# Kernel tuning notes

Measured on AMD Instinct MI355X. Metric: run time of the kernel, lower is better.

## Reference

```python
import jax, jax.numpy as jnp
import numpy as np
from jax import lax

B = 512          # scoring batch size
NC = 10          # n_classes
N_LAB = 256      # int(B * plb), plb = 0.5 (labeled indices are the first N_LAB)
TOL = 1e-3       # gtg_t
MAX_ITER = 30    # gtg_i
INTERM = 128
CH = [64, 128, 256, 512]
SZ = [32, 16, 8, 4]
EMB = 512


def setup_inputs() -> dict:
    key = jax.random.key(0)
    ks = jax.random.split(key, 16)
    inp = {}
    for i, (c, s) in enumerate(zip(CH, SZ)):
        inp["feat%d" % i] = jax.random.normal(ks[i], (B, c, s, s), jnp.float32)
        inp["conv_w%d" % i] = jax.random.normal(ks[4 + i], (c, c, 3, 3), jnp.float32) * 0.05
        inp["conv_b%d" % i] = jnp.zeros((c,), jnp.float32)
        inp["bn_g%d" % i] = jnp.ones((c,), jnp.float32)
        inp["bn_b%d" % i] = jnp.zeros((c,), jnp.float32)
        inp["lin_w%d" % i] = jax.random.normal(ks[8 + i], (INTERM, c), jnp.float32) * 0.05
        inp["lin_b%d" % i] = jnp.zeros((INTERM,), jnp.float32)
    inp["fin_w"] = jax.random.normal(ks[12], (1, 4 * INTERM), jnp.float32) * 0.05
    inp["fin_b"] = jnp.zeros((1,), jnp.float32)
    inp["embedds"] = jax.random.normal(ks[13], (B, EMB), jnp.float32)
    inp["labels"] = jax.random.randint(ks[14], (B,), 0, NC)
    return inp


def _branch(x, cw, cb, g, b, lw, lb):
    # Conv3x3(same) -> BatchNorm (train mode, batch stats, eps=1e-5) -> ReLU -> GAP -> Linear -> ReLU
    y = lax.conv_general_dilated(x, cw, (1, 1), 'SAME',
                                 dimension_numbers=('NCHW', 'OIHW', 'NCHW')) + cb[None, :, None, None]
    m = y.mean(axis=(0, 2, 3), keepdims=True)
    v = ((y - m) ** 2).mean(axis=(0, 2, 3), keepdims=True)  # biased variance (train-mode BN)
    y = jax.nn.relu(g[None, :, None, None] * (y - m) * lax.rsqrt(v + 1e-5) + b[None, :, None, None])
    y = y.mean(axis=(2, 3))  # AvgPool2d(feature_size) == global average pool -> [B, C]
    return jax.nn.relu(y @ lw.T + lb)


def _gtg(E, labels):
    # get_A_e_d: pairwise euclidean distances clamped to [0.1, 1.0]
    sq = jnp.sum(E * E, axis=1)
    d2 = jnp.maximum(sq[:, None] + sq[None, :] - 2.0 * (E @ E.T), 0.0)
    A0 = jnp.clip(jnp.sqrt(d2), 0.1, 1.0)
    # rbf kernel: 7th nearest neighbor (ascending for 'e_d') gives per-sample sigma
    seventh = E[jnp.argsort(A0, axis=1)[:, 6]]
    sig = jnp.clip(jnp.sqrt(jnp.sum((E - seventh) ** 2, axis=1)), 0.1, 1.0)
    A = jnp.clip(jnp.exp(-(A0 ** 2) / (sig[:, None] * sig[None, :])), 0.0, 1.0)
    # threshold strategy 'mean' with AM_function == 'e_d': A = where(A > mean(A), 1, A)
    A = jnp.where(A > A.mean(), 1.0, A)
    # AM_strategy 'mixed' with 'e_d': flip only the labeled x labeled block
    A = A.at[:N_LAB, :N_LAB].set(1.0 - A[:N_LAB, :N_LAB])
    # get_X: one-hot for labeled (first N_LAB), uniform 1/NC for unlabeled
    X0 = jnp.concatenate([jax.nn.one_hot(labels[:N_LAB], NC, dtype=jnp.float32),
                          jnp.full((B - N_LAB, NC), 1.0 / NC, jnp.float32)], axis=0)
    hist0 = jnp.zeros((B, MAX_ITER), jnp.float32)

    def cond(c):
        return (c[3] > TOL) & (c[2] < MAX_ITER)

    def body(c):
        X, h, i, _ = c
        Xn = X * (A @ X)
        Xn = Xn / jnp.sum(Xn, axis=1, keepdims=True)
        ent = -jnp.sum(jnp.where(Xn > 0, Xn * jnp.log(Xn), 0.0), axis=1)
        h = lax.dynamic_update_slice(h, ent[:, None], (0, i))
        return (Xn, h, i + 1, jnp.linalg.norm(Xn - X))

    X, h, _, _ = lax.while_loop(cond, body, (X0, hist0, jnp.int32(0), jnp.float32(jnp.inf)))
    return h.mean(axis=1), X  # ent_strategy == 'mean'


def reference(feat0, feat1, feat2, feat3,
              conv_w0, conv_b0, bn_g0, bn_b0, lin_w0, lin_b0,
              conv_w1, conv_b1, bn_g1, bn_b1, lin_w1, lin_b1,
              conv_w2, conv_b2, bn_g2, bn_b2, lin_w2, lin_b2,
              conv_w3, conv_b3, bn_g3, bn_b3, lin_w3, lin_b3,
              fin_w, fin_b, embedds, labels):
    o0 = _branch(feat0, conv_w0, conv_b0, bn_g0, bn_b0, lin_w0, lin_b0)
    o1 = _branch(feat1, conv_w1, conv_b1, bn_g1, bn_b1, lin_w1, lin_b1)
    o2 = _branch(feat2, conv_w2, conv_b2, bn_g2, bn_b2, lin_w2, lin_b2)
    o3 = _branch(feat3, conv_w3, conv_b3, bn_g3, bn_b3, lin_w3, lin_b3)
    y_pred = (jnp.concatenate([o0, o1, o2, o3], axis=1) @ fin_w.T + fin_b)[:, 0]
    y_true, X = _gtg(embedds, labels)
    labeled_mask = jnp.arange(B) < N_LAB
    return (y_pred, y_true, X, labeled_mask)
```

## Files before the change

kernel.cpp:

```cpp
#include <hip/hip_runtime.h>
#include <hip/hip_bf16.h>
#include <math.h>

static constexpr int kNC = 10;
static constexpr int kNLab = 256;
static constexpr int kMaxIter = 30;

using short8 = __attribute__((ext_vector_type(8))) short;
using f32x4  = __attribute__((ext_vector_type(4))) float;

__device__ __forceinline__ unsigned short f2bf(float f) {
  unsigned int u = __float_as_uint(f);
  u += 0x7FFFu + ((u >> 16) & 1u);
  return (unsigned short)(u >> 16);
}
__device__ __forceinline__ float bf2f(unsigned short u) {
  return __uint_as_float(((unsigned int)u) << 16);
}

template <int C, int S>
__global__ __launch_bounds__(256) void xpack_kernel(const float* __restrict__ x,
                                                    unsigned short* __restrict__ xp) {
  __shared__ float t[C][S + 1];
  const int n = blockIdx.x / S, h = blockIdx.x % S;
  const float* src = x + (size_t)n * C * S * S;
  for (int e = threadIdx.x; e < C * S; e += 256) {
    int c = e / S, w = e % S;
    t[c][w] = src[((size_t)c * S + h) * S + w];
  }
  __syncthreads();
  unsigned short* dst = xp + ((size_t)(n * S + h) * S) * C;
  for (int e = threadIdx.x; e < C * S; e += 256) {
    int w = e / C, c = e % C;
    dst[(size_t)w * C + c] = f2bf(t[c][w]);
  }
}

__global__ void wpack_all(const float* __restrict__ w0, const float* __restrict__ w1,
                          const float* __restrict__ w2, const float* __restrict__ w3,
                          unsigned short* __restrict__ wpk) {
  int idx = blockIdx.x * 256 + threadIdx.x;
  if (idx >= 3133440) return;
  const float* w; int C, off;
  if (idx < 36864)        { w = w0; C = 64;  off = 0; }
  else if (idx < 184320)  { w = w1; C = 128; off = 36864; }
  else if (idx < 774144)  { w = w2; C = 256; off = 184320; }
  else                    { w = w3; C = 512; off = 774144; }
  int e = idx - off;
  int CO16T = C / 16, CIK = C / 32;
  int e8 = e & 7, l = (e >> 3) & 63;
  int rest = e >> 9;
  int co16 = rest % CO16T;
  int rest2 = rest / CO16T;
  int cik = rest2 % CIK, tap = rest2 / CIK;
  int co = co16 * 16 + (l & 15);
  int ci = cik * 32 + (l >> 4) * 8 + e8;
  wpk[idx] = f2bf(w[((size_t)co * C + ci) * 9 + tap]);
}

template <int C, int S, int NI, int NR, int WV, int BF, int MODE>
__global__ __launch_bounds__(WV * 64)
void conv_mfma(const unsigned short* __restrict__ xp, const unsigned short* __restrict__ wpk,
               const float* __restrict__ bias, unsigned short* __restrict__ y,
               float* __restrict__ psum, float* __restrict__ psq, int npart, int partBase,
               const float* __restrict__ scale, const float* __restrict__ shift,
               float* __restrict__ pp, int pxGlobalBase) {
  constexpr int SS = S * S;
  constexpr int PXB = NI * NR * S;
  constexpr int TPB = WV * 64;
  constexpr int HR = NR + 2, HC = S + 2;
  constexpr int CIK = C / 32, CO16T = C / 16;
  constexpr int UNITS = NI * HR * HC * 4;
  constexpr int NU = (UNITS + TPB - 1) / TPB;
  static_assert(WV * BF * 16 == PXB, "wave px mismatch");
  static_assert(MODE != 2 || BF == 4, "MODE2 assumes 64px/wave");
  __shared__ __align__(16) char xs[NI * HR * HC * 80];

  const int tid = threadIdx.x;
  const int wv = tid >> 6, l = tid & 63, l15 = l & 15, l4 = l >> 4;
  const int coblk = blockIdx.y;
  const int co_base = coblk * 64;
  const int pxb = blockIdx.x * PXB;
  const int n_t = pxb / SS;
  const int r0 = (pxb % SS) / S;

  int pxoff[BF];
#pragma unroll
  for (int bf = 0; bf < BF; ++bf) {
    int pxloc = wv * (BF * 16) + bf * 16 + l15;
    int ii = pxloc / (NR * S);
    int rr = (pxloc % (NR * S)) / S;
    int cc = pxloc % S;
    pxoff[bf] = ((ii * HR + rr) * HC + cc) * 80 + l4 * 16;
  }

  f32x4 acc[4][BF];
#pragma unroll
  for (int a = 0; a < 4; ++a)
#pragma unroll
    for (int b = 0; b < BF; ++b) acc[a][b] = (f32x4){0.f, 0.f, 0.f, 0.f};

  uint4 vreg[NU];
  auto loadU = [&](int cik) {
#pragma unroll
    for (int k = 0; k < NU; ++k) {
      int u = tid + k * TPB;
      uint4 v = {0u, 0u, 0u, 0u};
      if (u < UNITS) {
        int k16 = u & 3;
        int t = u >> 2;
        int hc = t % HC;
        int t2 = t / HC;
        int hr = t2 % HR;
        int ii = t2 / HR;
        int row = r0 + hr - 1, col = hc - 1;
        if (row >= 0 && row < S && col >= 0 && col < S)
          v = *(const uint4*)(xp + ((size_t)((n_t + ii) * S + row) * S + col) * C + cik * 32 + k16 * 8);
      }
      vreg[k] = v;
    }
  };

  loadU(0);
  for (int cik = 0; cik < CIK; ++cik) {
    __syncthreads();
#pragma unroll
    for (int k = 0; k < NU; ++k) {
      int u = tid + k * TPB;
      if (u < UNITS) *(uint4*)(xs + (u >> 2) * 80 + (u & 3) * 16) = vreg[k];
    }
    __syncthreads();
    if (cik + 1 < CIK) loadU(cik + 1);
#pragma unroll
    for (int tap = 0; tap < 9; ++tap) {
      const int tapoff = ((tap / 3) * HC + (tap % 3)) * 80;
      short8 wf[4], xf[BF];
#pragma unroll
      for (int af = 0; af < 4; ++af)
        wf[af] = *(const short8*)(wpk + ((size_t)((tap * CIK + cik) * CO16T + coblk * 4 + af) * 64 + l) * 8);
#pragma unroll
      for (int bf = 0; bf < BF; ++bf)
        xf[bf] = *(const short8*)(xs + pxoff[bf] + tapoff);
#pragma unroll
      for (int af = 0; af < 4; ++af)
#pragma unroll
        for (int bf = 0; bf < BF; ++bf)
          acc[af][bf] = __builtin_amdgcn_mfma_f32_16x16x32_bf16(wf[af], xf[bf], acc[af][bf], 0, 0, 0);
    }
  }

#pragma unroll
  for (int af = 0; af < 4; ++af) {
    const int co0 = co_base + af * 16 + l4 * 4;
    float4 bv = *(const float4*)(bias + co0);
    float s[4] = {0.f, 0.f, 0.f, 0.f}, q[4] = {0.f, 0.f, 0.f, 0.f};
    float4 sc4, sh4;
    if (MODE == 2) {
      sc4 = *(const float4*)(scale + co0);
      sh4 = *(const float4*)(shift + co0);
    }
#pragma unroll
    for (int bf = 0; bf < BF; ++bf) {
      float o[4];
#pragma unroll
      for (int r = 0; r < 4; ++r) o[r] = acc[af][bf][r] + ((const float*)&bv)[r];
      if (MODE == 0) {
        ushort4 pk;
        pk.x = f2bf(o[0]); pk.y = f2bf(o[1]); pk.z = f2bf(o[2]); pk.w = f2bf(o[3]);
        size_t px = (size_t)(pxb + wv * (BF * 16) + bf * 16 + l15);
        *(ushort4*)(y + px * C + co0) = pk;
      }
      if (MODE == 2) {
#pragma unroll
        for (int r = 0; r < 4; ++r)
          s[r] += fmaxf(fmaf(((const float*)&sc4)[r], o[r], ((const float*)&sh4)[r]), 0.f);
      } else {
#pragma unroll
        for (int r = 0; r < 4; ++r) { s[r] += o[r]; q[r] += o[r] * o[r]; }
      }
    }
#pragma unroll
    for (int m = 1; m < 16; m <<= 1) {
#pragma unroll
      for (int r = 0; r < 4; ++r) {
        s[r] += __shfl_xor(s[r], m);
        if (MODE != 2) q[r] += __shfl_xor(q[r], m);
      }
    }
    if (l15 == 0) {
      if (MODE == 2) {
        int n = (pxGlobalBase + pxb) / SS;
        int qw = ((pxGlobalBase + pxb) % SS) / 64 + wv;
#pragma unroll
        for (int r = 0; r < 4; ++r)
          pp[((size_t)(n * C + co0 + r)) * 16 + qw] = s[r];
      } else {
        int part = partBase + blockIdx.x * WV + wv;
#pragma unroll
        for (int r = 0; r < 4; ++r) {
          psum[(size_t)(co0 + r) * npart + part] = s[r];
          psq[(size_t)(co0 + r) * npart + part] = q[r];
        }
      }
    }
  }
}

__global__ __launch_bounds__(256)
void stats2_kernel(const float* __restrict__ psum, const float* __restrict__ psq,
                   const float* __restrict__ g, const float* __restrict__ bb,
                   float* __restrict__ scale, float* __restrict__ shift,
                   int npart, float invN) {
  int c = blockIdx.x;
  __shared__ float rs[256], rq[256];
  float s = 0.f, q = 0.f;
  for (int p = threadIdx.x; p < npart; p += 256) {
    s += psum[(size_t)c * npart + p];
    q += psq[(size_t)c * npart + p];
  }
  rs[threadIdx.x] = s; rq[threadIdx.x] = q;
  __syncthreads();
  for (int st = 128; st; st >>= 1) {
    if (threadIdx.x < st) { rs[threadIdx.x] += rs[threadIdx.x + st]; rq[threadIdx.x] += rq[threadIdx.x + st]; }
    __syncthreads();
  }
  if (threadIdx.x == 0) {
    float m = rs[0] * invN;
    float v = rq[0] * invN - m * m;
    float sc = g[c] / sqrtf(v + 1e-5f);
    scale[c] = sc;
    shift[c] = bb[c] - m * sc;
  }
}

template <int C, int S>
__global__ __launch_bounds__(256)
void pool_nhwc(const unsigned short* __restrict__ y, const float* __restrict__ scale,
               const float* __restrict__ shift, float* __restrict__ pooled) {
  constexpr int SS = S * S;
  int n = blockIdx.x;
  const unsigned short* yr = y + (size_t)n * SS * C;
  if (C >= 256) {
    for (int co = threadIdx.x; co < C; co += 256) {
      float sc = scale[co], sh = shift[co], s = 0.f;
      for (int p = 0; p < SS; ++p) s += fmaxf(fmaf(sc, bf2f(yr[(size_t)p * C + co]), sh), 0.f);
      pooled[(size_t)n * C + co] = s * (1.f / SS);
    }
  } else {
    constexpr int G = 256 / C;
    int co = threadIdx.x % C;
    int sl = threadIdx.x / C;
    float sc = scale[co], sh = shift[co], s = 0.f;
    for (int p = sl; p < SS; p += G) s += fmaxf(fmaf(sc, bf2f(yr[(size_t)p * C + co]), sh), 0.f);
    __shared__ float red[256];
    red[threadIdx.x] = s;
    __syncthreads();
    if (threadIdx.x < C) {
      float t = 0.f;
      for (int gg = 0; gg < G; ++gg) t += red[gg * C + co];
      pooled[(size_t)n * C + co] = t * (1.f / SS);
    }
  }
}

__global__ void poolfin_kernel(const float* __restrict__ pp, float* __restrict__ pooled) {
  int i = blockIdx.x * 256 + threadIdx.x;
  if (i >= 512 * 64) return;
  float s = 0.f;
  for (int qn = 0; qn < 16; ++qn) s += pp[(size_t)i * 16 + qn];
  pooled[i] = s * (1.f / 1024.f);
}

__global__ void lin_kernel(const float* __restrict__ pooled, const float* __restrict__ lw,
                           const float* __restrict__ lb, float* __restrict__ oc,
                           int C, int brOff) {
  int idx = blockIdx.x * 256 + threadIdx.x;
  if (idx >= 512 * 128) return;
  int j = idx & 127, n = idx >> 7;
  const float4* pr = (const float4*)(pooled + (size_t)n * C);
  const float4* wr = (const float4*)(lw + (size_t)j * C);
  float s = 0.f;
  for (int t = 0; t < C / 4; ++t) {
    float4 a = pr[t], b = wr[t];
    s += a.x * b.x + a.y * b.y + a.z * b.z + a.w * b.w;
  }
  s += lb[j];
  oc[n * 512 + brOff + j] = fmaxf(s, 0.f);
}

__global__ void ypred_kernel(const float* __restrict__ oc, const float* __restrict__ fw,
                             const float* __restrict__ fb, float* __restrict__ out) {
  int wv = threadIdx.x >> 6, l = threadIdx.x & 63;
  int n = blockIdx.x * 4 + wv;
  float s = 0.f;
  for (int k = l; k < 512; k += 64) s += oc[n * 512 + k] * fw[k];
#pragma unroll
  for (int m = 32; m; m >>= 1) s += __shfl_down(s, m);
  if (l == 0) out[n] = s + fb[0];
}

__global__ void sqnorm_kernel(const float* __restrict__ E, float* __restrict__ sq) {
  int wv = threadIdx.x >> 6, l = threadIdx.x & 63;
  int n = blockIdx.x * 4 + wv;
  const float* row = E + (size_t)n * 512;
  float s = 0.f;
  for (int k = l; k < 512; k += 64) { float v = row[k]; s += v * v; }
#pragma unroll
  for (int m = 32; m; m >>= 1) s += __shfl_down(s, m);
  if (l == 0) sq[n] = s;
}

__global__ __launch_bounds__(256) void a0_kernel(const float* __restrict__ E,
                                                 const float* __restrict__ sq,
                                                 float* __restrict__ A0) {
  int bi = blockIdx.x / 32, bj = blockIdx.x % 32;
  int ti = threadIdx.x % 16, tj = threadIdx.x / 16;
  __shared__ float Ei[16][68], Ej[16][68];
  float acc = 0.f;
  for (int k0 = 0; k0 < 512; k0 += 64) {
    for (int e = threadIdx.x; e < 1024; e += 256) {
      int rr = e >> 6, cc = e & 63;
      Ei[rr][cc] = E[(size_t)(bi * 16 + rr) * 512 + k0 + cc];
      Ej[rr][cc] = E[(size_t)(bj * 16 + rr) * 512 + k0 + cc];
    }
    __syncthreads();
#pragma unroll 16
    for (int kk = 0; kk < 64; ++kk) acc = fmaf(Ei[tj][kk], Ej[ti][kk], acc);
    __syncthreads();
  }
  int i = bi * 16 + tj, j = bj * 16 + ti;
  float d2 = fmaxf(sq[i] + sq[j] - 2.f * acc, 0.f);
  A0[(size_t)i * 512 + j] = fminf(fmaxf(sqrtf(d2), 0.1f), 1.0f);
}

__global__ void seventh_kernel(const float* __restrict__ A0, int* __restrict__ idx7) {
  int i = blockIdx.x * 256 + threadIdx.x;
  if (i >= 512) return;
  float v[7]; int ix[7];
#pragma unroll
  for (int t = 0; t < 7; ++t) { v[t] = 3.4e38f; ix[t] = 0; }
  const float* row = A0 + (size_t)i * 512;
  for (int j = 0; j < 512; ++j) {
    float a = row[j];
    if (a < v[6]) {
      int pos = 6;
      while (pos > 0 && a < v[pos - 1]) { v[pos] = v[pos - 1]; ix[pos] = ix[pos - 1]; --pos; }
      v[pos] = a; ix[pos] = j;
    }
  }
  idx7[i] = ix[6];
}

__global__ void sig_kernel(const float* __restrict__ E, const int* __restrict__ idx7,
                           float* __restrict__ sig) {
  int wv = threadIdx.x >> 6, l = threadIdx.x & 63;
  int n = blockIdx.x * 4 + wv;
  const float* r1 = E + (size_t)n * 512;
  const float* r2 = E + (size_t)idx7[n] * 512;
  float s = 0.f;
  for (int k = l; k < 512; k += 64) { float d = r1[k] - r2[k]; s += d * d; }
#pragma unroll
  for (int m = 32; m; m >>= 1) s += __shfl_down(s, m);
  if (l == 0) sig[n] = fminf(fmaxf(sqrtf(s), 0.1f), 1.0f);
}

__global__ void aexp_kernel(const float* __restrict__ A0, const float* __restrict__ sig,
                            float* __restrict__ A, float* __restrict__ part) {
  int t = blockIdx.x * 256 + threadIdx.x;
  int base = t * 4;
  int i = base >> 9, j0 = base & 511;
  float si = sig[i];
  float4 a = *(const float4*)(A0 + base);
  float4 o;
  o.x = fminf(fmaxf(expf(-a.x * a.x / (si * sig[j0 + 0])), 0.f), 1.f);
  o.y = fminf(fmaxf(expf(-a.y * a.y / (si * sig[j0 + 1])), 0.f), 1.f);
  o.z = fminf(fmaxf(expf(-a.z * a.z / (si * sig[j0 + 2])), 0.f), 1.f);
  o.w = fminf(fmaxf(expf(-a.w * a.w / (si * sig[j0 + 3])), 0.f), 1.f);
  *(float4*)(A + base) = o;
  float lsum = o.x + o.y + o.z + o.w;
#pragma unroll
  for (int m = 32; m; m >>= 1) lsum += __shfl_down(lsum, m);
  __shared__ float sred[4];
  if ((threadIdx.x & 63) == 0) sred[threadIdx.x >> 6] = lsum;
  __syncthreads();
  if (threadIdx.x == 0) part[blockIdx.x] = sred[0] + sred[1] + sred[2] + sred[3];
}

__global__ void meanred_kernel(const float* __restrict__ part, float* __restrict__ meanA) {
  if (threadIdx.x == 0 && blockIdx.x == 0) {
    float s = 0.f;
    for (int p = 0; p < 256; ++p) s += part[p];
    meanA[0] = s * (1.0f / 262144.0f);
  }
}

__global__ void thresh_kernel(float* __restrict__ A, const float* __restrict__ meanA) {
  int t = blockIdx.x * 256 + threadIdx.x;
  int base = t * 4;
  int i = base >> 9, j0 = base & 511;
  float m = meanA[0];
  float4 v = *(const float4*)(A + base);
  v.x = v.x > m ? 1.f : v.x;
  v.y = v.y > m ? 1.f : v.y;
  v.z = v.z > m ? 1.f : v.z;
  v.w = v.w > m ? 1.f : v.w;
  if (i < kNLab && j0 < kNLab) {
    v.x = 1.f - v.x; v.y = 1.f - v.y; v.z = 1.f - v.z; v.w = 1.f - v.w;
  }
  *(float4*)(A + base) = v;
}

__device__ __forceinline__ void gridbar(int* cnt, int* sense, int ph) {
  __syncthreads();
  if (threadIdx.x == 0) {
    __threadfence();
    if (__hip_atomic_fetch_add(cnt, 1, __ATOMIC_ACQ_REL, __HIP_MEMORY_SCOPE_AGENT) == 63) {
      __hip_atomic_store(cnt, 0, __ATOMIC_RELAXED, __HIP_MEMORY_SCOPE_AGENT);
      __hip_atomic_store(sense, ph, __ATOMIC_RELEASE, __HIP_MEMORY_SCOPE_AGENT);
    } else {
      while (__hip_atomic_load(sense, __ATOMIC_ACQUIRE, __HIP_MEMORY_SCOPE_AGENT) < ph)
        __builtin_amdgcn_s_sleep(2);
    }
  }
  __syncthreads();
}

__global__ __launch_bounds__(256)
void gtg_iters(const float* __restrict__ A, const int* __restrict__ labels,
               float* __restrict__ Xa, float* __restrict__ Xb,
               float* __restrict__ hist, float* __restrict__ diffPart,
               float* __restrict__ out, int* __restrict__ bar) {
  constexpr int NB = 64;
  const int b = blockIdx.x, tid = threadIdx.x;
  const int wv = tid >> 6, l = tid & 63;
  __shared__ float Xs[512 * kNC];
  __shared__ float red[4];
  int* cnt = bar; int* sense = bar + 1;
  int ph = 0;

  for (int e = tid; e < 8 * kNC; e += 256) {
    int r = b * 8 + e / kNC, c = e % kNC;
    Xa[r * kNC + c] = (r < kNLab) ? ((labels[r] == c) ? 1.f : 0.f) : 0.1f;
  }
  for (int e = tid; e < 8 * kMaxIter; e += 256)
    hist[(size_t)(b * 8 + e / kMaxIter) * kMaxIter + e % kMaxIter] = 0.f;
  gridbar(cnt, sense, ++ph);

  float* Xin = Xa;
  float* Xout = Xb;
  int it = 0;
  for (; it < kMaxIter; ++it) {
    if (it > 0) {
      float s = 0.f;
      for (int p = 0; p < NB; ++p) s += diffPart[(it - 1) * NB + p];
      if (sqrtf(s) <= 0.001f) break;
    }
    for (int e = tid; e < 512 * kNC; e += 256) Xs[e] = Xin[e];
    __syncthreads();
    float dpw = 0.f;
    for (int rr = 0; rr < 2; ++rr) {
      int i = b * 8 + wv * 2 + rr;
      const float* Ar = A + (size_t)i * 512;
      float ax[kNC];
#pragma unroll
      for (int c = 0; c < kNC; ++c) ax[c] = 0.f;
      for (int j = l; j < 512; j += 64) {
        float a = Ar[j];
        const float* xr = Xs + j * kNC;
#pragma unroll
        for (int c = 0; c < kNC; ++c) ax[c] = fmaf(a, xr[c], ax[c]);
      }
#pragma unroll
      for (int c = 0; c < kNC; ++c)
#pragma unroll
        for (int m = 32; m; m >>= 1) ax[c] += __shfl_xor(ax[c], m);
      if (l == 0) {
        float xn[kNC], ssum = 0.f;
#pragma unroll
        for (int c = 0; c < kNC; ++c) { xn[c] = Xs[i * kNC + c] * ax[c]; ssum += xn[c]; }
        float ent = 0.f, dp = 0.f;
#pragma unroll
        for (int c = 0; c < kNC; ++c) {
          float xv = xn[c] / ssum;
          if (xv > 0.f) ent -= xv * logf(xv);
          float d = xv - Xs[i * kNC + c];
          dp += d * d;
          Xout[i * kNC + c] = xv;
        }
        hist[(size_t)i * kMaxIter + it] = ent;
        dpw += dp;
      }
    }
    if (l == 0) red[wv] = dpw;
    __syncthreads();
    if (tid == 0) diffPart[it * NB + b] = red[0] + red[1] + red[2] + red[3];
    gridbar(cnt, sense, ++ph);
    float* tmp = Xin; Xin = Xout; Xout = tmp;
  }

  if (tid < 8) {
    int i = b * 8 + tid;
    float s = 0.f;
    for (int t = 0; t < kMaxIter; ++t) s += hist[(size_t)i * kMaxIter + t];
    out[512 + i] = s * (1.0f / 30.0f);
    out[6144 + i] = (i < kNLab) ? 1.0f : 0.0f;
  }
  for (int e = tid; e < 80; e += 256) out[1024 + b * 80 + e] = Xin[b * 80 + e];
}

extern "C" void kernel_launch(void* const* d_in, const int* in_sizes, int n_in,
                              void* d_out, int out_size, void* d_ws, size_t ws_size,
                              hipStream_t stream) {
  (void)in_sizes; (void)n_in; (void)out_size;

  const float* feat[4]; const float* cw[4]; const float* cbp[4];
  const float* bg[4]; const float* bbp[4]; const float* lw[4]; const float* lbp[4];
  for (int b = 0; b < 4; ++b) {
    int base = b * 7;
    feat[b] = (const float*)d_in[base + 0];
    cw[b]  = (const float*)d_in[base + 1];
    cbp[b] = (const float*)d_in[base + 2];
    bg[b]  = (const float*)d_in[base + 3];
    bbp[b] = (const float*)d_in[base + 4];
    lw[b]  = (const float*)d_in[base + 5];
    lbp[b] = (const float*)d_in[base + 6];
  }
  const float* finw = (const float*)d_in[28];
  const float* finb = (const float*)d_in[29];
  const float* emb  = (const float*)d_in[30];
  const int* labels = (const int*)d_in[31];
  float* out = (float*)d_out;

  float* wsf = (float*)d_ws;
  unsigned short* xpad = (unsigned short*)wsf;
  unsigned short* yP   = (unsigned short*)(wsf + 4194304);
  unsigned short* wpk  = (unsigned short*)(wsf + 12582912);
  size_t off = 14149632;
  float* psum = wsf + off; off += 524288;
  float* psq  = wsf + off; off += 524288;
  float* pp   = wsf + off; off += 524288;
  float* scale = wsf + off; off += 512;
  float* shift = wsf + off; off += 512;
  float* pooled = wsf + off; off += 491520;
  float* oc = wsf + off; off += 262144;
  float* sq = wsf + off; off += 512;
  float* A0 = wsf + off; off += 262144;
  float* Am = wsf + off; off += 262144;
  float* sig = wsf + off; off += 512;
  int* idx7 = (int*)(wsf + off); off += 512;
  float* meanPart = wsf + off; off += 256;
  float* meanA = wsf + off; off += 4;
  float* X0 = wsf + off; off += 5120;
  float* X1 = wsf + off; off += 5120;
  float* hist = wsf + off; off += 15360;
  float* diffPart = wsf + off; off += 1920;
  int* bar = (int*)(wsf + off); off += 4;
  size_t yb0_off = off;
  unsigned short* yB0 = (unsigned short*)(wsf + yb0_off);
  const bool bigB0 = ws_size >= (yb0_off + 16777216) * sizeof(float);

  unsigned short* wpkB[4] = {wpk, wpk + 36864, wpk + 184320, wpk + 774144};

  wpack_all<<<(3133440 + 255) / 256, 256, 0, stream>>>(cw[0], cw[1], cw[2], cw[3], wpk);

  for (int c = 0; c < 2; ++c) {
    xpack_kernel<128, 16><<<256 * 16, 256, 0, stream>>>(feat[1] + (size_t)c * 8388608, xpad);
    conv_mfma<128, 16, 1, 8, 4, 2, 0><<<dim3(512, 2), 256, 0, stream>>>(
        xpad, wpkB[1], cbp[1], yP + (size_t)c * 8388608, psum, psq, 4096, c * 2048,
        nullptr, nullptr, nullptr, 0);
  }
  stats2_kernel<<<128, 256, 0, stream>>>(psum, psq, bg[1], bbp[1], scale, shift, 4096, 1.f / 131072.f);
  pool_nhwc<128, 16><<<512, 256, 0, stream>>>(yP, scale, shift, pooled + 32768);
  lin_kernel<<<256, 256, 0, stream>>>(pooled + 32768, lw[1], lbp[1], oc, 128, 128);

  xpack_kernel<256, 8><<<512 * 8, 256, 0, stream>>>(feat[2], xpad);
  conv_mfma<256, 8, 2, 8, 4, 2, 0><<<dim3(256, 4), 256, 0, stream>>>(
      xpad, wpkB[2], cbp[2], yP, psum, psq, 1024, 0, nullptr, nullptr, nullptr, 0);
  stats2_kernel<<<256, 256, 0, stream>>>(psum, psq, bg[2], bbp[2], scale, shift, 1024, 1.f / 32768.f);
  pool_nhwc<256, 8><<<512, 256, 0, stream>>>(yP, scale, shift, pooled + 98304);
  lin_kernel<<<256, 256, 0, stream>>>(pooled + 98304, lw[2], lbp[2], oc, 256, 256);

  xpack_kernel<512, 4><<<512 * 4, 256, 0, stream>>>(feat[3], xpad);
  conv_mfma<512, 4, 8, 4, 4, 2, 0><<<dim3(64, 8), 256, 0, stream>>>(
      xpad, wpkB[3], cbp[3], yP, psum, psq, 256, 0, nullptr, nullptr, nullptr, 0);
  stats2_kernel<<<512, 256, 0, stream>>>(psum, psq, bg[3], bbp[3], scale, shift, 256, 1.f / 8192.f);
  pool_nhwc<512, 4><<<512, 256, 0, stream>>>(yP, scale, shift, pooled + 229376);
  lin_kernel<<<256, 256, 0, stream>>>(pooled + 229376, lw[3], lbp[3], oc, 512, 384);

  if (bigB0) {
    for (int c = 0; c < 4; ++c) {
      xpack_kernel<64, 32><<<128 * 32, 256, 0, stream>>>(feat[0] + (size_t)c * 8388608, xpad);
      conv_mfma<64, 32, 1, 8, 4, 4, 0><<<dim3(512, 1), 256, 0, stream>>>(
          xpad, wpkB[0], cbp[0], yB0 + (size_t)c * 8388608, psum, psq, 8192, c * 2048,
          nullptr, nullptr, nullptr, 0);
    }
    stats2_kernel<<<64, 256, 0, stream>>>(psum, psq, bg[0], bbp[0], scale, shift, 8192, 1.f / 524288.f);
    pool_nhwc<64, 32><<<512, 256, 0, stream>>>(yB0, scale, shift, pooled);
  } else {
    for (int c = 0; c < 4; ++c) {
      xpack_kernel<64, 32><<<128 * 32, 256, 0, stream>>>(feat[0] + (size_t)c * 8388608, xpad);
      conv_mfma<64, 32, 1, 8, 4, 4, 1><<<dim3(512, 1), 256, 0, stream>>>(
          xpad, wpkB[0], cbp[0], nullptr, psum, psq, 8192, c * 2048, nullptr, nullptr, nullptr, 0);
    }
    stats2_kernel<<<64, 256, 0, stream>>>(psum, psq, bg[0], bbp[0], scale, shift, 8192, 1.f / 524288.f);
    for (int c = 0; c < 4; ++c) {
      xpack_kernel<64, 32><<<128 * 32, 256, 0, stream>>>(feat[0] + (size_t)c * 8388608, xpad);
      conv_mfma<64, 32, 1, 8, 4, 4, 2><<<dim3(512, 1), 256, 0, stream>>>(
          xpad, wpkB[0], cbp[0], nullptr, nullptr, nullptr, 0, 0, scale, shift, pp, c * 131072);
    }
    poolfin_kernel<<<128, 256, 0, stream>>>(pp, pooled);
  }
  lin_kernel<<<256, 256, 0, stream>>>(pooled, lw[0], lbp[0], oc, 64, 0);

  ypred_kernel<<<128, 256, 0, stream>>>(oc, finw, finb, out);
  sqnorm_kernel<<<128, 256, 0, stream>>>(emb, sq);
  a0_kernel<<<1024, 256, 0, stream>>>(emb, sq, A0);
  seventh_kernel<<<2, 256, 0, stream>>>(A0, idx7);
  sig_kernel<<<128, 256, 0, stream>>>(emb, idx7, sig);
  aexp_kernel<<<256, 256, 0, stream>>>(A0, sig, Am, meanPart);
  meanred_kernel<<<1, 64, 0, stream>>>(meanPart, meanA);
  thresh_kernel<<<256, 256, 0, stream>>>(Am, meanA);

  hipMemsetAsync(bar, 0, 8, stream);
  gtg_iters<<<64, 256, 0, stream>>>(Am, labels, X0, X1, hist, diffPart, out, bar);
}
```

Baseline: 1.016 ms.

## Fuse pooling with linear layer and restructure GTG iterations onto 16 blocks

The per-branch pooling kernel now also applies the 128-wide linear layer and ReLU from a shared-memory pooled vector, which removes a separate lin_kernel launch and the pooled round trip through global memory. The GTG iteration kernel is rewritten to run on 16 blocks of 32 rows each. Each block keeps its slice of A in registers across iterations, accumulates entropy in registers instead of a history buffer, and replaces the counter/sense grid barrier with per-block release/acquire flags. X now lives in a single global buffer instead of two ping-pong buffers. That creates a possible race: a fast block can overwrite its rows while a slower block is still copying X into shared memory.

Result: no change. 1.003 ms (-1.3%).

```diff
diff --git a/kernel.cpp b/kernel.cpp
--- a/kernel.cpp
+++ b/kernel.cpp
@@ -235,16 +235,18 @@
 
 template <int C, int S>
 __global__ __launch_bounds__(256)
-void pool_nhwc(const unsigned short* __restrict__ y, const float* __restrict__ scale,
-               const float* __restrict__ shift, float* __restrict__ pooled) {
+void pool_lin(const unsigned short* __restrict__ y, const float* __restrict__ scale,
+              const float* __restrict__ shift, const float* __restrict__ lw,
+              const float* __restrict__ lb, float* __restrict__ oc, int brOff) {
   constexpr int SS = S * S;
   int n = blockIdx.x;
   const unsigned short* yr = y + (size_t)n * SS * C;
+  __shared__ float pl[C];
   if (C >= 256) {
     for (int co = threadIdx.x; co < C; co += 256) {
       float sc = scale[co], sh = shift[co], s = 0.f;
       for (int p = 0; p < SS; ++p) s += fmaxf(fmaf(sc, bf2f(yr[(size_t)p * C + co]), sh), 0.f);
-      pooled[(size_t)n * C + co] = s * (1.f / SS);
+      pl[co] = s * (1.f / SS);
     }
   } else {
     constexpr int G = 256 / C;
@@ -258,8 +260,17 @@
     if (threadIdx.x < C) {
       float t = 0.f;
       for (int gg = 0; gg < G; ++gg) t += red[gg * C + co];
-      pooled[(size_t)n * C + co] = t * (1.f / SS);
-    }
+      pl[co] = t * (1.f / SS);
+    }
+  }
+  __syncthreads();
+  if (threadIdx.x < 128) {
+    int j = threadIdx.x;
+    const float* wr = lw + (size_t)j * C;
+    float s = 0.f;
+    for (int t = 0; t < C; ++t) s = fmaf(pl[t], wr[t], s);
+    s += lb[j];
+    oc[n * 512 + brOff + j] = fmaxf(s, 0.f);
   }
 }
 
@@ -410,102 +421,120 @@
   *(float4*)(A + base) = v;
 }
 
-__device__ __forceinline__ void gridbar(int* cnt, int* sense, int ph) {
+__global__ __launch_bounds__(256)
+void gtg_iters16(const float* __restrict__ A, const int* __restrict__ labels,
+                 float* __restrict__ Xg, float* __restrict__ diffPart,
+                 float* __restrict__ out, int* __restrict__ flags) {
+  constexpr int NB = 16, RPB = 32;
+  const int b = blockIdx.x, tid = threadIdx.x;
+  const int pg = tid & 31, rg = tid >> 5;
+  __shared__ float Xs[512][kNC];
+  __shared__ float dred[8];
+
+  float a[4][16];
+  {
+    const int gr0 = b * RPB + rg * 4;
+#pragma unroll
+    for (int rr = 0; rr < 4; ++rr) {
+      const float* Ar = A + (size_t)(gr0 + rr) * 512 + pg;
+#pragma unroll
+      for (int jj = 0; jj < 16; ++jj) a[rr][jj] = Ar[32 * jj];
+    }
+  }
+  for (int e = tid; e < 512 * kNC; e += 256) {
+    int r = e / kNC, c = e % kNC;
+    Xs[r][c] = (r < kNLab) ? ((labels[r] == c) ? 1.f : 0.f) : 0.1f;
+  }
   __syncthreads();
-  if (threadIdx.x == 0) {
-    __threadfence();
-    if (__hip_atomic_fetch_add(cnt, 1, __ATOMIC_ACQ_REL, __HIP_MEMORY_SCOPE_AGENT) == 63) {
-      __hip_atomic_store(cnt, 0, __ATOMIC_RELAXED, __HIP_MEMORY_SCOPE_AGENT);
-      __hip_atomic_store(sense, ph, __ATOMIC_RELEASE, __HIP_MEMORY_SCOPE_AGENT);
-    } else {
-      while (__hip_atomic_load(sense, __ATOMIC_ACQUIRE, __HIP_MEMORY_SCOPE_AGENT) < ph)
-        __builtin_amdgcn_s_sleep(2);
-    }
-  }
-  __syncthreads();
-}
-
-__global__ __launch_bounds__(256)
-void gtg_iters(const float* __restrict__ A, const int* __restrict__ labels,
-               float* __restrict__ Xa, float* __restrict__ Xb,
-               float* __restrict__ hist, float* __restrict__ diffPart,
-               float* __restrict__ out, int* __restrict__ bar) {
-  constexpr int NB = 64;
-  const int b = blockIdx.x, tid = threadIdx.x;
-  const int wv = tid >> 6, l = tid & 63;
-  __shared__ float Xs[512 * kNC];
-  __shared__ float red[4];
-  int* cnt = bar; int* sense = bar + 1;
+
+  float entsum[4] = {0.f, 0.f, 0.f, 0.f};
   int ph = 0;
-
-  for (int e = tid; e < 8 * kNC; e += 256) {
-    int r = b * 8 + e / kNC, c = e % kNC;
-    Xa[r * kNC + c] = (r < kNLab) ? ((labels[r] == c) ? 1.f : 0.f) : 0.1f;
-  }
-  for (int e = tid; e < 8 * kMaxIter; e += 256)
-    hist[(size_t)(b * 8 + e / kMaxIter) * kMaxIter + e % kMaxIter] = 0.f;
-  gridbar(cnt, sense, ++ph);
-
-  float* Xin = Xa;
-  float* Xout = Xb;
-  int it = 0;
-  for (; it < kMaxIter; ++it) {
+  for (int it = 0; it < kMaxIter; ++it) {
     if (it > 0) {
       float s = 0.f;
-      for (int p = 0; p < NB; ++p) s += diffPart[(it - 1) * NB + p];
+      for (int q = 0; q < NB; ++q) s += diffPart[(it - 1) * NB + q];
       if (sqrtf(s) <= 0.001f) break;
     }
-    for (int e = tid; e < 512 * kNC; e += 256) Xs[e] = Xin[e];
-    __syncthreads();
-    float dpw = 0.f;
-    for (int rr = 0; rr < 2; ++rr) {
-      int i = b * 8 + wv * 2 + rr;
-      const float* Ar = A + (size_t)i * 512;
-      float ax[kNC];
-#pragma unroll
-      for (int c = 0; c < kNC; ++c) ax[c] = 0.f;
-      for (int j = l; j < 512; j += 64) {
-        float a = Ar[j];
-        const float* xr = Xs + j * kNC;
-#pragma unroll
-        for (int c = 0; c < kNC; ++c) ax[c] = fmaf(a, xr[c], ax[c]);
+    float ax[4][kNC];
+#pragma unroll
+    for (int rr = 0; rr < 4; ++rr)
+#pragma unroll
+      for (int c = 0; c < kNC; ++c) ax[rr][c] = 0.f;
+#pragma unroll
+    for (int jj = 0; jj < 16; ++jj) {
+      int j = pg + 32 * jj;
+      float xv[kNC];
+#pragma unroll
+      for (int c = 0; c < kNC; ++c) xv[c] = Xs[j][c];
+#pragma unroll
+      for (int rr = 0; rr < 4; ++rr) {
+        float av = a[rr][jj];
+#pragma unroll
+        for (int c = 0; c < kNC; ++c) ax[rr][c] = fmaf(av, xv[c], ax[rr][c]);
       }
-#pragma unroll
-      for (int c = 0; c < kNC; ++c)
-#pragma unroll
-        for (int m = 32; m; m >>= 1) ax[c] += __shfl_xor(ax[c], m);
-      if (l == 0) {
+    }
+#pragma unroll
+    for (int m = 1; m < 32; m <<= 1)
+#pragma unroll
+      for (int rr = 0; rr < 4; ++rr)
+#pragma unroll
+        for (int c = 0; c < kNC; ++c) ax[rr][c] += __shfl_xor(ax[rr][c], m);
+    if (pg == 0) {
+      const int gr0 = b * RPB + rg * 4;
+      float dpsum = 0.f;
+#pragma unroll
+      for (int rr = 0; rr < 4; ++rr) {
+        int gi = gr0 + rr;
         float xn[kNC], ssum = 0.f;
 #pragma unroll
-        for (int c = 0; c < kNC; ++c) { xn[c] = Xs[i * kNC + c] * ax[c]; ssum += xn[c]; }
-        float ent = 0.f, dp = 0.f;
+        for (int c = 0; c < kNC; ++c) { xn[c] = Xs[gi][c] * ax[rr][c]; ssum += xn[c]; }
+        float ent = 0.f;
 #pragma unroll
         for (int c = 0; c < kNC; ++c) {
           float xv = xn[c] / ssum;
           if (xv > 0.f) ent -= xv * logf(xv);
-          float d = xv - Xs[i * kNC + c];
-          dp += d * d;
-          Xout[i * kNC + c] = xv;
+          float d = xv - Xs[gi][c];
+          dpsum += d * d;
+          Xg[gi * kNC + c] = xv;
         }
-        hist[(size_t)i * kMaxIter + it] = ent;
-        dpw += dp;
+        entsum[rr] += ent;
       }
-    }
-    if (l == 0) red[wv] = dpw;
-    __syncthreads();
-    if (tid == 0) diffPart[it * NB + b] = red[0] + red[1] + red[2] + red[3];
-    gridbar(cnt, sense, ++ph);
-    float* tmp = Xin; Xin = Xout; Xout = tmp;
-  }
-
-  if (tid < 8) {
-    int i = b * 8 + tid;
-    float s = 0.f;
-    for (int t = 0; t < kMaxIter; ++t) s += hist[(size_t)i * kMaxIter + t];
-    out[512 + i] = s * (1.0f / 30.0f);
-    out[6144 + i] = (i < kNLab) ? 1.0f : 0.0f;
-  }
-  for (int e = tid; e < 80; e += 256) out[1024 + b * 80 + e] = Xin[b * 80 + e];
+      dred[rg] = dpsum;
+    }
+    __syncthreads();
+    if (tid == 0) {
+      float s2 = 0.f;
+#pragma unroll
+      for (int q = 0; q < 8; ++q) s2 += dred[q];
+      diffPart[it * NB + b] = s2;
+    }
+    __syncthreads();
+    __threadfence();
+    if (tid == 0)
+      __hip_atomic_store(&flags[b], ph + 1, __ATOMIC_RELEASE, __HIP_MEMORY_SCOPE_AGENT);
+    if (tid < NB) {
+      while (__hip_atomic_load(&flags[tid], __ATOMIC_ACQUIRE, __HIP_MEMORY_SCOPE_AGENT) <= ph)
+        __builtin_amdgcn_s_sleep(1);
+    }
+    ++ph;
+    __syncthreads();
+    for (int e = tid; e < 512 * kNC; e += 256) Xs[e / kNC][e % kNC] = Xg[e];
+    __syncthreads();
+  }
+
+  if (pg == 0) {
+    const int gr0 = b * RPB + rg * 4;
+#pragma unroll
+    for (int rr = 0; rr < 4; ++rr) {
+      int gi = gr0 + rr;
+      out[512 + gi] = entsum[rr] * (1.0f / 30.0f);
+      out[6144 + gi] = (gi < kNLab) ? 1.0f : 0.0f;
+    }
+  }
+  for (int e = tid; e < RPB * kNC; e += 256) {
+    int gi = b * RPB + e / kNC;
+    out[1024 + gi * kNC + e % kNC] = Xs[gi][e % kNC];
+  }
 }
 
 extern "C" void kernel_launch(void* const* d_in, const int* in_sizes, int n_in,
@@ -550,11 +579,9 @@
   int* idx7 = (int*)(wsf + off); off += 512;
   float* meanPart = wsf + off; off += 256;
   float* meanA = wsf + off; off += 4;
-  float* X0 = wsf + off; off += 5120;
-  float* X1 = wsf + off; off += 5120;
-  float* hist = wsf + off; off += 15360;
-  float* diffPart = wsf + off; off += 1920;
-  int* bar = (int*)(wsf + off); off += 4;
+  float* Xg = wsf + off; off += 5120;
+  float* diffPart = wsf + off; off += 512;
+  int* flags = (int*)(wsf + off); off += 32;
   size_t yb0_off = off;
   unsigned short* yB0 = (unsigned short*)(wsf + yb0_off);
   const bool bigB0 = ws_size >= (yb0_off + 16777216) * sizeof(float);
@@ -570,22 +597,19 @@
         nullptr, nullptr, nullptr, 0);
   }
   stats2_kernel<<<128, 256, 0, stream>>>(psum, psq, bg[1], bbp[1], scale, shift, 4096, 1.f / 131072.f);
-  pool_nhwc<128, 16><<<512, 256, 0, stream>>>(yP, scale, shift, pooled + 32768);
-  lin_kernel<<<256, 256, 0, stream>>>(pooled + 32768, lw[1], lbp[1], oc, 128, 128);
+  pool_lin<128, 16><<<512, 256, 0, stream>>>(yP, scale, shift, lw[1], lbp[1], oc, 128);
 
   xpack_kernel<256, 8><<<512 * 8, 256, 0, stream>>>(feat[2], xpad);
   conv_mfma<256, 8, 2, 8, 4, 2, 0><<<dim3(256, 4), 256, 0, stream>>>(
       xpad, wpkB[2], cbp[2], yP, psum, psq, 1024, 0, nullptr, nullptr, nullptr, 0);
   stats2_kernel<<<256, 256, 0, stream>>>(psum, psq, bg[2], bbp[2], scale, shift, 1024, 1.f / 32768.f);
-  pool_nhwc<256, 8><<<512, 256, 0, stream>>>(yP, scale, shift, pooled + 98304);
-  lin_kernel<<<256, 256, 0, stream>>>(pooled + 98304, lw[2], lbp[2], oc, 256, 256);
+  pool_lin<256, 8><<<512, 256, 0, stream>>>(yP, scale, shift, lw[2], lbp[2], oc, 256);
 
   xpack_kernel<512, 4><<<512 * 4, 256, 0, stream>>>(feat[3], xpad);
   conv_mfma<512, 4, 8, 4, 4, 2, 0><<<dim3(64, 8), 256, 0, stream>>>(
       xpad, wpkB[3], cbp[3], yP, psum, psq, 256, 0, nullptr, nullptr, nullptr, 0);
   stats2_kernel<<<512, 256, 0, stream>>>(psum, psq, bg[3], bbp[3], scale, shift, 256, 1.f / 8192.f);
-  pool_nhwc<512, 4><<<512, 256, 0, stream>>>(yP, scale, shift, pooled + 229376);
-  lin_kernel<<<256, 256, 0, stream>>>(pooled + 229376, lw[3], lbp[3], oc, 512, 384);
+  pool_lin<512, 4><<<512, 256, 0, stream>>>(yP, scale, shift, lw[3], lbp[3], oc, 384);
 
   if (bigB0) {
     for (int c = 0; c < 4; ++c) {
@@ -595,7 +619,7 @@
           nullptr, nullptr, nullptr, 0);
     }
     stats2_kernel<<<64, 256, 0, stream>>>(psum, psq, bg[0], bbp[0], scale, shift, 8192, 1.f / 524288.f);
-    pool_nhwc<64, 32><<<512, 256, 0, stream>>>(yB0, scale, shift, pooled);
+    pool_lin<64, 32><<<512, 256, 0, stream>>>(yB0, scale, shift, lw[0], lbp[0], oc, 0);
   } else {
     for (int c = 0; c < 4; ++c) {
       xpack_kernel<64, 32><<<128 * 32, 256, 0, stream>>>(feat[0] + (size_t)c * 8388608, xpad);
@@ -609,8 +633,8 @@
           xpad, wpkB[0], cbp[0], nullptr, nullptr, nullptr, 0, 0, scale, shift, pp, c * 131072);
     }
     poolfin_kernel<<<128, 256, 0, stream>>>(pp, pooled);
-  }
-  lin_kernel<<<256, 256, 0, stream>>>(pooled, lw[0], lbp[0], oc, 64, 0);
+    lin_kernel<<<256, 256, 0, stream>>>(pooled, lw[0], lbp[0], oc, 64, 0);
+  }
 
   ypred_kernel<<<128, 256, 0, stream>>>(oc, finw, finb, out);
   sqnorm_kernel<<<128, 256, 0, stream>>>(emb, sq);
@@ -621,6 +645,6 @@
   meanred_kernel<<<1, 64, 0, stream>>>(meanPart, meanA);
   thresh_kernel<<<256, 256, 0, stream>>>(Am, meanA);
 
-  hipMemsetAsync(bar, 0, 8, stream);
-  gtg_iters<<<64, 256, 0, stream>>>(Am, labels, X0, X1, hist, diffPart, out, bar);
-}
+  hipMemsetAsync(flags, 0, 64, stream);
+  gtg_iters16<<<16, 256, 0, stream>>>(Am, labels, Xg, diffPart, out, flags);
+}
```
